# Kernel tuning notes

Measured on AMD Instinct MI355X. Metric: run time of the kernel, lower is better.

## Reference

```python
import jax, jax.numpy as jnp
import numpy as np

RADIUS = 2.0
DECAY = 1.0


def setup_inputs() -> dict:
    key = jax.random.key(0)
    k1, k2 = jax.random.split(key)
    x = jax.random.normal(k1, (2048, 16), dtype=jnp.float32)
    data = jax.random.normal(k2, (65536, 16), dtype=jnp.float32)
    return {"x": x, "data": data}


def reference(x, data):
    # Brute-force L2 nearest-neighbor (faiss IndexFlatL2 / IVF nlist=1 == exact search)
    # dist2[q, n] = ||x_q - data_n||^2, via the expansion trick.
    x2 = jnp.sum(x * x, axis=1, keepdims=True)            # [Nq, 1]
    d2 = jnp.sum(data * data, axis=1)                      # [Nd]
    dist2 = x2 + d2[None, :] - 2.0 * (x @ data.T)          # [Nq, Nd] -- dominant traffic
    nn2 = jnp.maximum(jnp.min(dist2, axis=1), 0.0)         # clamp tiny negatives from cancellation
    dist = jnp.sqrt(jnp.maximum(nn2, 1e-12))               # sqrt of squared L2, squeeze(k=1)

    # bump_above(dist, RADIUS, DECAY):
    #   inside mask: exp(decay / (d^2 - r^2)) / exp(-decay / r^2)
    #   outside: 0
    r2 = RADIUS * RADIUS
    mask = jnp.abs(dist) < RADIUS
    denom = jnp.where(mask, dist * dist - r2, -1.0)        # safe denom outside mask
    bump = jnp.where(mask, jnp.exp(DECAY / denom + DECAY / r2), 0.0)
    return bump
```

## Files before the change

kernel.cpp:

```cpp
#include <hip/hip_runtime.h>
#include <float.h>
#include <math.h>

constexpr int NQ = 2048;
constexpr int ND = 65536;
constexpr int D  = 16;

constexpr int SCH   = 64;
constexpr int CP    = ND / SCH;
constexpr int TPW   = CP / 32;

constexpr unsigned LDS_BYTES = 65536 + 4096;

typedef short bf16x8 __attribute__((ext_vector_type(8)));
typedef float f32x16 __attribute__((ext_vector_type(16)));

__device__ __forceinline__ unsigned short f2bf(float f) {
    unsigned u = __float_as_uint(f);
    u += 0x7FFFu + ((u >> 16) & 1u);
    return (unsigned short)(u >> 16);
}
__device__ __forceinline__ float bf2f(unsigned short h) {
    return __uint_as_float(((unsigned)h) << 16);
}

__global__ __launch_bounds__(256, 2) void knn_mfma(const float* __restrict__ x,
                                                   const float* __restrict__ data,
                                                   float* __restrict__ part) {
    const int lb  = blockIdx.x;
    const int xcd = lb & 7;
    const int rr  = lb >> 3;
    const int qx  = rr & 7;
    const int cg  = rr >> 3;
    const int cy  = xcd + 8 * cg;

    const int tid  = threadIdx.x;
    const int w    = tid >> 6;
    const int l    = tid & 63;
    const int half = l >> 5;
    const int n31  = l & 31;
    const int qbase = qx * 256 + w * 64;
    const int pbase = cy * CP;

    extern __shared__ __align__(16) char smem[];
    unsigned short* sP = (unsigned short*)smem;
    float*          sN = (float*)(smem + 65536);

#pragma unroll
    for (int j = 0; j < 4; ++j) {
        const int pl = j * 256 + tid;
        const float4* r4 = (const float4*)(data + (size_t)(pbase + pl) * D);
        float4 a = r4[0], b = r4[1], c = r4[2], e = r4[3];
        float v[16] = {a.x, a.y, a.z, a.w, b.x, b.y, b.z, b.w,
                       c.x, c.y, c.z, c.w, e.x, e.y, e.z, e.w};
        unsigned short hi[16], lo[16];
        float n = 0.f;
#pragma unroll
        for (int k = 0; k < 16; ++k) {
            n = fmaf(v[k], v[k], n);
            unsigned short h = f2bf(v[k]);
            hi[k] = h;
            lo[k] = f2bf(v[k] - bf2f(h));
        }
        const int t  = pl >> 5;
        const int cc = pl & 31;
        unsigned short* tb = sP + t * 1024;
        const uint4* h4 = (const uint4*)hi;
        const uint4* l4 = (const uint4*)lo;
        *(uint4*)(tb +       cc * 8) = h4[0];
        *(uint4*)(tb + 256 + cc * 8) = h4[1];
        *(uint4*)(tb + 512 + cc * 8) = l4[0];
        *(uint4*)(tb + 768 + cc * 8) = l4[1];
        sN[pl] = -0.5f * n;
    }

    bf16x8 axh0, axl0, axh1, axl1;
    {
        const float* xr0 = x + (size_t)(qbase + n31) * D + half * 8;
        float4 a0 = *(const float4*)xr0;
        float4 a1 = *(const float4*)(xr0 + 4);
        const float xv0[8] = {a0.x, a0.y, a0.z, a0.w, a1.x, a1.y, a1.z, a1.w};
#pragma unroll
        for (int k = 0; k < 8; ++k) {
            unsigned short h = f2bf(xv0[k]);
            axh0[k] = (short)h;
            axl0[k] = (short)f2bf(xv0[k] - bf2f(h));
        }
        const float* xr1 = x + (size_t)(qbase + 32 + n31) * D + half * 8;
        float4 b0 = *(const float4*)xr1;
        float4 b1 = *(const float4*)(xr1 + 4);
        const float xv1[8] = {b0.x, b0.y, b0.z, b0.w, b1.x, b1.y, b1.z, b1.w};
#pragma unroll
        for (int k = 0; k < 8; ++k) {
            unsigned short h = f2bf(xv1[k]);
            axh1[k] = (short)h;
            axl1[k] = (short)f2bf(xv1[k] - bf2f(h));
        }
    }

    __syncthreads();

    const unsigned short* lp  = sP + l * 8;
    const float*          lnp = sN + n31;
#define LDH(t) (*(const bf16x8*)(lp + (size_t)(t) * 1024))
#define LDL(t) (*(const bf16x8*)(lp + (size_t)(t) * 1024 + 512))
#define LDN(t) (lnp[(t) * 32])

    f32x16 rbest0, rbest1;
#pragma unroll
    for (int r = 0; r < 16; ++r) { rbest0[r] = -FLT_MAX; rbest1[r] = -FLT_MAX; }

    auto compute_pair = [&](bf16x8 h0, bf16x8 l0, float n0,
                            bf16x8 h1, bf16x8 l1, float n1) {
        f32x16 c00, c01, c10, c11;
#pragma unroll
        for (int r = 0; r < 16; ++r) {
            c00[r] = n0; c01[r] = n1; c10[r] = n0; c11[r] = n1;
        }
        c00 = __builtin_amdgcn_mfma_f32_32x32x16_bf16(axh0, h0, c00, 0, 0, 0);
        c01 = __builtin_amdgcn_mfma_f32_32x32x16_bf16(axh0, h1, c01, 0, 0, 0);
        c10 = __builtin_amdgcn_mfma_f32_32x32x16_bf16(axh1, h0, c10, 0, 0, 0);
        c11 = __builtin_amdgcn_mfma_f32_32x32x16_bf16(axh1, h1, c11, 0, 0, 0);
        c00 = __builtin_amdgcn_mfma_f32_32x32x16_bf16(axl0, h0, c00, 0, 0, 0);
        c01 = __builtin_amdgcn_mfma_f32_32x32x16_bf16(axl0, h1, c01, 0, 0, 0);
        c10 = __builtin_amdgcn_mfma_f32_32x32x16_bf16(axl1, h0, c10, 0, 0, 0);
        c11 = __builtin_amdgcn_mfma_f32_32x32x16_bf16(axl1, h1, c11, 0, 0, 0);
        c00 = __builtin_amdgcn_mfma_f32_32x32x16_bf16(axh0, l0, c00, 0, 0, 0);
        c01 = __builtin_amdgcn_mfma_f32_32x32x16_bf16(axh0, l1, c01, 0, 0, 0);
        c10 = __builtin_amdgcn_mfma_f32_32x32x16_bf16(axh1, l0, c10, 0, 0, 0);
        c11 = __builtin_amdgcn_mfma_f32_32x32x16_bf16(axh1, l1, c11, 0, 0, 0);
#pragma unroll
        for (int r = 0; r < 16; ++r) {
            rbest0[r] = fmaxf(rbest0[r], fmaxf(c00[r], c01[r]));
            rbest1[r] = fmaxf(rbest1[r], fmaxf(c10[r], c11[r]));
        }
    };

    for (int p = 0; p < TPW; p += 2) {
        compute_pair(LDH(p),     LDL(p),     LDN(p),
                     LDH(p + 1), LDL(p + 1), LDN(p + 1));
    }
#undef LDH
#undef LDL
#undef LDN

#pragma unroll
    for (int r = 0; r < 16; ++r) {
        float v0 = rbest0[r];
        v0 = fmaxf(v0, __shfl_xor(v0, 1, 32));
        v0 = fmaxf(v0, __shfl_xor(v0, 2, 32));
        v0 = fmaxf(v0, __shfl_xor(v0, 4, 32));
        v0 = fmaxf(v0, __shfl_xor(v0, 8, 32));
        v0 = fmaxf(v0, __shfl_xor(v0, 16, 32));
        rbest0[r] = v0;
        float v1 = rbest1[r];
        v1 = fmaxf(v1, __shfl_xor(v1, 1, 32));
        v1 = fmaxf(v1, __shfl_xor(v1, 2, 32));
        v1 = fmaxf(v1, __shfl_xor(v1, 4, 32));
        v1 = fmaxf(v1, __shfl_xor(v1, 8, 32));
        v1 = fmaxf(v1, __shfl_xor(v1, 16, 32));
        rbest1[r] = v1;
    }
    if (n31 == 0) {
        float* pp = part + (size_t)cy * NQ + qbase + 4 * half;
#pragma unroll
        for (int r = 0; r < 16; ++r) pp[(r & 3) + 8 * (r >> 2)] = rbest0[r];
        pp += 32;
#pragma unroll
        for (int r = 0; r < 16; ++r) pp[(r & 3) + 8 * (r >> 2)] = rbest1[r];
    }
}

__global__ __launch_bounds__(256) void knn_final(const float* __restrict__ x,
                                                 const float* __restrict__ part,
                                                 float* __restrict__ out) {
    const int q = blockIdx.x * 256 + threadIdx.x;
    const float4* xr = (const float4*)(x + (size_t)q * D);
    float4 a = xr[0], b = xr[1], c = xr[2], e = xr[3];
    float x2 = a.x * a.x;
    x2 = fmaf(a.y, a.y, x2); x2 = fmaf(a.z, a.z, x2); x2 = fmaf(a.w, a.w, x2);
    x2 = fmaf(b.x, b.x, x2); x2 = fmaf(b.y, b.y, x2); x2 = fmaf(b.z, b.z, x2); x2 = fmaf(b.w, b.w, x2);
    x2 = fmaf(c.x, c.x, x2); x2 = fmaf(c.y, c.y, x2); x2 = fmaf(c.z, c.z, x2); x2 = fmaf(c.w, c.w, x2);
    x2 = fmaf(e.x, e.x, x2); x2 = fmaf(e.y, e.y, x2); x2 = fmaf(e.z, e.z, x2); x2 = fmaf(e.w, e.w, x2);

    float mbest = -FLT_MAX;
#pragma unroll
    for (int cI = 0; cI < SCH; ++cI) mbest = fmaxf(mbest, part[(size_t)cI * NQ + q]);

    float nn2  = fmaxf(fmaf(-2.f, mbest, x2), 0.f);
    float dist = sqrtf(fmaxf(nn2, 1e-12f));
    float bump = 0.f;
    if (dist < 2.0f) {
        float denom = dist * dist - 4.0f;
        bump = expf(1.0f / denom + 0.25f);
    }
    out[q] = bump;
}

__global__ __launch_bounds__(256) void neg_half_norms(const float* __restrict__ data,
                                                      float* __restrict__ nhn) {
    const int p = blockIdx.x * 256 + threadIdx.x;
    const float4* r = (const float4*)(data + (size_t)p * D);
    float4 a = r[0], b = r[1], c = r[2], e = r[3];
    float n = a.x * a.x;
    n = fmaf(a.y, a.y, n); n = fmaf(a.z, a.z, n); n = fmaf(a.w, a.w, n);
    n = fmaf(b.x, b.x, n); n = fmaf(b.y, b.y, n); n = fmaf(b.z, b.z, n); n = fmaf(b.w, b.w, n);
    n = fmaf(c.x, c.x, n); n = fmaf(c.y, c.y, n); n = fmaf(c.z, c.z, n); n = fmaf(c.w, c.w, n);
    n = fmaf(e.x, e.x, n); n = fmaf(e.y, e.y, n); n = fmaf(e.z, e.z, n); n = fmaf(e.w, e.w, n);
    nhn[p] = -0.5f * n;
}

__global__ __launch_bounds__(256) void knn_partial_fb(const float* __restrict__ x,
                                                      const float* __restrict__ data,
                                                      const float* __restrict__ nhn,
                                                      float* __restrict__ part, int cp) {
    const int q     = blockIdx.x * 256 + threadIdx.x;
    const int pbase = blockIdx.y * cp;
    const float4* xr = (const float4*)(x + (size_t)q * D);
    const float4 xa = xr[0], xb = xr[1], xc = xr[2], xd = xr[3];
    const float* dp = data + (size_t)pbase * D;
    const float* np = nhn + pbase;
    float best = -FLT_MAX;
    for (int i = 0; i < cp; i += 4) {
#pragma unroll
        for (int j = 0; j < 4; ++j) {
            const float* r  = dp + (size_t)(i + j) * D;
            const float  hn = np[i + j];
            float ca = xa.x * r[0];
            ca = fmaf(xa.y, r[1], ca);  ca = fmaf(xa.z, r[2], ca);  ca = fmaf(xa.w, r[3], ca);
            ca = fmaf(xb.x, r[4], ca);  ca = fmaf(xb.y, r[5], ca);  ca = fmaf(xb.z, r[6], ca);
            ca = fmaf(xb.w, r[7], ca);
            float cb = fmaf(xc.x, r[8], hn);
            cb = fmaf(xc.y, r[9],  cb); cb = fmaf(xc.z, r[10], cb); cb = fmaf(xc.w, r[11], cb);
            cb = fmaf(xd.x, r[12], cb); cb = fmaf(xd.y, r[13], cb); cb = fmaf(xd.z, r[14], cb);
            cb = fmaf(xd.w, r[15], cb);
            best = fmaxf(best, ca + cb);
        }
    }
    part[(size_t)blockIdx.y * NQ + q] = best;
}

__global__ __launch_bounds__(256) void knn_final_fb(const float* __restrict__ x,
                                                    const float* __restrict__ part,
                                                    float* __restrict__ out, int S) {
    const int q = blockIdx.x * 256 + threadIdx.x;
    const float4* xr = (const float4*)(x + (size_t)q * D);
    float4 a = xr[0], b = xr[1], c = xr[2], e = xr[3];
    float x2 = a.x * a.x;
    x2 = fmaf(a.y, a.y, x2); x2 = fmaf(a.z, a.z, x2); x2 = fmaf(a.w, a.w, x2);
    x2 = fmaf(b.x, b.x, x2); x2 = fmaf(b.y, b.y, x2); x2 = fmaf(b.z, b.z, x2); x2 = fmaf(b.w, b.w, x2);
    x2 = fmaf(c.x, c.x, x2); x2 = fmaf(c.y, c.y, x2); x2 = fmaf(c.z, c.z, x2); x2 = fmaf(c.w, c.w, x2);
    x2 = fmaf(e.x, e.x, x2); x2 = fmaf(e.y, e.y, x2); x2 = fmaf(e.z, e.z, x2); x2 = fmaf(e.w, e.w, x2);
    float mb = -FLT_MAX;
    for (int cI = 0; cI < S; ++cI) mb = fmaxf(mb, part[(size_t)cI * NQ + q]);
    float nn2  = fmaxf(fmaf(-2.f, mb, x2), 0.f);
    float dist = sqrtf(fmaxf(nn2, 1e-12f));
    float bump = 0.f;
    if (dist < 2.0f) {
        float denom = dist * dist - 4.0f;
        bump = expf(1.0f / denom + 0.25f);
    }
    out[q] = bump;
}

extern "C" void kernel_launch(void* const* d_in, const int* in_sizes, int n_in,
                              void* d_out, int out_size, void* d_ws, size_t ws_size,
                              hipStream_t stream) {
    const float* x    = (const float*)d_in[0];
    const float* data = (const float*)d_in[1];
    float* out = (float*)d_out;

    const size_t needed = (size_t)SCH * NQ * 4;

    if (ws_size >= needed) {
        float* part = (float*)d_ws;
        knn_mfma<<<8 * SCH, 256, LDS_BYTES, stream>>>(x, data, part);
        knn_final<<<NQ / 256, 256, 0, stream>>>(x, part, out);
    } else {
        int S = 32;
        while (S > 1 && (size_t)(ND + S * NQ) * sizeof(float) > ws_size) S >>= 1;
        const int cp = ND / S;
        float* nhn  = (float*)d_ws;
        float* part = (float*)d_ws + ND;
        neg_half_norms<<<ND / 256, 256, 0, stream>>>(data, nhn);
        knn_partial_fb<<<dim3(NQ / 256, S), 256, 0, stream>>>(x, data, nhn, part, cp);
        knn_final_fb<<<NQ / 256, 256, 0, stream>>>(x, part, out, S);
    }
}
```

Before: 74.04 us.

## Double data chunks, halve per-block LDS, and split MFMA pair to cut register pressure

```diff
diff --git a/kernel.cpp b/kernel.cpp
--- a/kernel.cpp
+++ b/kernel.cpp
@@ -6,11 +6,11 @@
 constexpr int ND = 65536;
 constexpr int D  = 16;
 
-constexpr int SCH   = 64;
+constexpr int SCH   = 128;
 constexpr int CP    = ND / SCH;
 constexpr int TPW   = CP / 32;
 
-constexpr unsigned LDS_BYTES = 65536 + 4096;
+constexpr unsigned LDS_BYTES = 32768 + 2048;
 
 typedef short bf16x8 __attribute__((ext_vector_type(8)));
 typedef float f32x16 __attribute__((ext_vector_type(16)));
@@ -24,9 +24,9 @@
     return __uint_as_float(((unsigned)h) << 16);
 }
 
-__global__ __launch_bounds__(256, 2) void knn_mfma(const float* __restrict__ x,
-                                                   const float* __restrict__ data,
-                                                   float* __restrict__ part) {
+__global__ __launch_bounds__(256) void knn_mfma(const float* __restrict__ x,
+                                                const float* __restrict__ data,
+                                                float* __restrict__ part) {
     const int lb  = blockIdx.x;
     const int xcd = lb & 7;
     const int rr  = lb >> 3;
@@ -44,10 +44,10 @@
 
     extern __shared__ __align__(16) char smem[];
     unsigned short* sP = (unsigned short*)smem;
-    float*          sN = (float*)(smem + 65536);
-
-#pragma unroll
-    for (int j = 0; j < 4; ++j) {
+    float*          sN = (float*)(smem + 32768);
+
+#pragma unroll
+    for (int j = 0; j < 2; ++j) {
         const int pl = j * 256 + tid;
         const float4* r4 = (const float4*)(data + (size_t)(pbase + pl) * D);
         float4 a = r4[0], b = r4[1], c = r4[2], e = r4[3];
@@ -110,35 +110,38 @@
 #pragma unroll
     for (int r = 0; r < 16; ++r) { rbest0[r] = -FLT_MAX; rbest1[r] = -FLT_MAX; }
 
-    auto compute_pair = [&](bf16x8 h0, bf16x8 l0, float n0,
-                            bf16x8 h1, bf16x8 l1, float n1) {
-        f32x16 c00, c01, c10, c11;
-#pragma unroll
-        for (int r = 0; r < 16; ++r) {
-            c00[r] = n0; c01[r] = n1; c10[r] = n0; c11[r] = n1;
-        }
-        c00 = __builtin_amdgcn_mfma_f32_32x32x16_bf16(axh0, h0, c00, 0, 0, 0);
-        c01 = __builtin_amdgcn_mfma_f32_32x32x16_bf16(axh0, h1, c01, 0, 0, 0);
-        c10 = __builtin_amdgcn_mfma_f32_32x32x16_bf16(axh1, h0, c10, 0, 0, 0);
-        c11 = __builtin_amdgcn_mfma_f32_32x32x16_bf16(axh1, h1, c11, 0, 0, 0);
-        c00 = __builtin_amdgcn_mfma_f32_32x32x16_bf16(axl0, h0, c00, 0, 0, 0);
-        c01 = __builtin_amdgcn_mfma_f32_32x32x16_bf16(axl0, h1, c01, 0, 0, 0);
-        c10 = __builtin_amdgcn_mfma_f32_32x32x16_bf16(axl1, h0, c10, 0, 0, 0);
-        c11 = __builtin_amdgcn_mfma_f32_32x32x16_bf16(axl1, h1, c11, 0, 0, 0);
-        c00 = __builtin_amdgcn_mfma_f32_32x32x16_bf16(axh0, l0, c00, 0, 0, 0);
-        c01 = __builtin_amdgcn_mfma_f32_32x32x16_bf16(axh0, l1, c01, 0, 0, 0);
-        c10 = __builtin_amdgcn_mfma_f32_32x32x16_bf16(axh1, l0, c10, 0, 0, 0);
-        c11 = __builtin_amdgcn_mfma_f32_32x32x16_bf16(axh1, l1, c11, 0, 0, 0);
-#pragma unroll
-        for (int r = 0; r < 16; ++r) {
-            rbest0[r] = fmaxf(rbest0[r], fmaxf(c00[r], c01[r]));
-            rbest1[r] = fmaxf(rbest1[r], fmaxf(c10[r], c11[r]));
-        }
-    };
-
     for (int p = 0; p < TPW; p += 2) {
-        compute_pair(LDH(p),     LDL(p),     LDN(p),
-                     LDH(p + 1), LDL(p + 1), LDN(p + 1));
+        bf16x8 h0 = LDH(p),     l0 = LDL(p);
+        bf16x8 h1 = LDH(p + 1), l1 = LDL(p + 1);
+        float  n0 = LDN(p),     n1 = LDN(p + 1);
+        {
+            f32x16 c0, c1;
+#pragma unroll
+            for (int r = 0; r < 16; ++r) { c0[r] = n0; c1[r] = n1; }
+            c0 = __builtin_amdgcn_mfma_f32_32x32x16_bf16(axh0, h0, c0, 0, 0, 0);
+            c1 = __builtin_amdgcn_mfma_f32_32x32x16_bf16(axh0, h1, c1, 0, 0, 0);
+            c0 = __builtin_amdgcn_mfma_f32_32x32x16_bf16(axl0, h0, c0, 0, 0, 0);
+            c1 = __builtin_amdgcn_mfma_f32_32x32x16_bf16(axl0, h1, c1, 0, 0, 0);
+            c0 = __builtin_amdgcn_mfma_f32_32x32x16_bf16(axh0, l0, c0, 0, 0, 0);
+            c1 = __builtin_amdgcn_mfma_f32_32x32x16_bf16(axh0, l1, c1, 0, 0, 0);
+#pragma unroll
+            for (int r = 0; r < 16; ++r)
+                rbest0[r] = fmaxf(rbest0[r], fmaxf(c0[r], c1[r]));
+        }
+        {
+            f32x16 c0, c1;
+#pragma unroll
+            for (int r = 0; r < 16; ++r) { c0[r] = n0; c1[r] = n1; }
+            c0 = __builtin_amdgcn_mfma_f32_32x32x16_bf16(axh1, h0, c0, 0, 0, 0);
+            c1 = __builtin_amdgcn_mfma_f32_32x32x16_bf16(axh1, h1, c1, 0, 0, 0);
+            c0 = __builtin_amdgcn_mfma_f32_32x32x16_bf16(axl1, h0, c0, 0, 0, 0);
+            c1 = __builtin_amdgcn_mfma_f32_32x32x16_bf16(axl1, h1, c1, 0, 0, 0);
+            c0 = __builtin_amdgcn_mfma_f32_32x32x16_bf16(axh1, l0, c0, 0, 0, 0);
+            c1 = __builtin_amdgcn_mfma_f32_32x32x16_bf16(axh1, l1, c1, 0, 0, 0);
+#pragma unroll
+            for (int r = 0; r < 16; ++r)
+                rbest1[r] = fmaxf(rbest1[r], fmaxf(c0[r], c1[r]));
+        }
     }
 #undef LDH
 #undef LDL
```

Result: slower. 82.62 us (+11.6%).
